# Kernel optimization log

Measured on AMD Instinct MI355X. Metric: run time of the kernel, lower is better.

Reference implementation:

```python
import jax, jax.numpy as jnp
from jax import lax
import numpy as np

D = 1024
H = 16
DK = D // 2 // H   # 32 key head dim
DV = D // H        # 64 value head dim
GATE_NORM = 16.0
SCALE = DK ** (-0.5)
EPS = 1e-5


def setup_inputs() -> dict:
    key = jax.random.key(0)
    ks = jax.random.split(key, 10)
    s = 0.02
    return {
        "inputs": jax.random.normal(ks[0], (4, 4096, D), dtype=jnp.float32),
        "Wq": jax.random.normal(ks[1], (D, D // 2), dtype=jnp.float32) * s,
        "Wk": jax.random.normal(ks[2], (D, D // 2), dtype=jnp.float32) * s,
        "Wg1": jax.random.normal(ks[3], (D, 16), dtype=jnp.float32) * s,
        "Wg2": jax.random.normal(ks[4], (16, D // 2), dtype=jnp.float32) * s,
        "Wv": jax.random.normal(ks[5], (D, D), dtype=jnp.float32) * s,
        "Wg": jax.random.normal(ks[6], (D, D), dtype=jnp.float32) * s,
        "bg": jax.random.normal(ks[7], (D,), dtype=jnp.float32) * s,
        "Wo": jax.random.normal(ks[8], (D, D), dtype=jnp.float32) * s,
    }


def _split_heads(x, dh):
    # [B, L, H*dh] -> [B, H, L, dh]
    B, L, _ = x.shape
    return x.reshape(B, L, H, dh).transpose(0, 2, 1, 3)


def _gla_scan(q, k, v, log_gate):
    # q,k,log_gate: [B,H,L,DK]; v: [B,H,L,DV]
    B = q.shape[0]
    qt = jnp.moveaxis(q, 2, 0)          # [L,B,H,DK]
    kt = jnp.moveaxis(k, 2, 0)
    vt = jnp.moveaxis(v, 2, 0)          # [L,B,H,DV]
    gt = jnp.exp(jnp.moveaxis(log_gate, 2, 0))  # [L,B,H,DK]

    def step(state, inp):
        qq, kk, vv, gg = inp
        # state: [B,H,DK,DV]
        state = state * gg[..., None] + kk[..., :, None] * vv[..., None, :]
        out = jnp.einsum('bhd,bhde->bhe', qq, state)
        return state, out

    init = jnp.zeros((B, H, DK, DV), dtype=q.dtype)
    _, outs = lax.scan(step, init, (qt, kt, vt, gt))
    return jnp.moveaxis(outs, 0, 2)     # [B,H,L,DV]


def reference(inputs, Wq, Wk, Wg1, Wg2, Wv, Wg, bg, Wo):
    B, L, _ = inputs.shape
    q = _split_heads(inputs @ Wq, DK)
    k = _split_heads((inputs @ Wk) * SCALE, DK)
    kg = _split_heads((inputs @ Wg1) @ Wg2, DK)
    v = _split_heads(inputs @ Wv, DV)
    gate = jax.nn.silu(inputs @ Wg + bg)            # [B,L,D]

    log_gate = jax.nn.log_sigmoid(kg) / GATE_NORM
    o = _gla_scan(q, k, v, log_gate)                # [B,H,L,DV]

    # group norm over value head dim (no affine)
    mu = jnp.mean(o, axis=-1, keepdims=True)
    var = jnp.var(o, axis=-1, keepdims=True)
    o = (o - mu) * lax.rsqrt(var + EPS)

    o = o.transpose(0, 2, 1, 3).reshape(B, L, D)    # b h l d -> b l (h d)
    return (gate * o) @ Wo
```

## Files before the change

### kernel.cpp

```cpp
#include <hip/hip_runtime.h>
#include <cstdint>

namespace {

constexpr int Lq  = 4096;
constexpr int Bq  = 4;
constexpr int H_  = 16;
constexpr int Mrows = Bq * Lq;
constexpr int CHK  = 64;
constexpr int NCHK = Lq / CHK;
constexpr int QKVS = 3072;
constexpr float kScale = 0.17677669529663687f;
constexpr float kEps   = 1e-5f;

typedef __attribute__((ext_vector_type(8))) short short8;
typedef __attribute__((ext_vector_type(4))) float f32x4;

__device__ __forceinline__ float bf2f(unsigned short u) {
  return __uint_as_float(((unsigned)u) << 16);
}
__device__ __forceinline__ unsigned short f2bf(float f) {
  unsigned u = __float_as_uint(f);
  u += 0x7fffu + ((u >> 16) & 1u);
  return (unsigned short)(u >> 16);
}
__device__ __forceinline__ void gload_lds16(const void* g, void* l) {
  __builtin_amdgcn_global_load_lds(
      (const __attribute__((address_space(1))) void*)g,
      (__attribute__((address_space(3))) void*)l, 16, 0, 0);
}

__global__ __launch_bounds__(256)
void cvt_bf16(const float* __restrict__ in, unsigned short* __restrict__ out, int n4)
{
  int i = blockIdx.x * 256 + threadIdx.x;
  const int stride = gridDim.x * 256;
  for (; i < n4; i += stride) {
    float4 f = ((const float4*)in)[i];
    ushort4 u = make_ushort4(f2bf(f.x), f2bf(f.y), f2bf(f.z), f2bf(f.w));
    ((ushort4*)out)[i] = u;
  }
}

struct CvtArgs {
  const float* W[5];
  unsigned short* Wt[5];
  int   N[5];
  float scale[5];
  int   start[5];
  int   nb[5];
};

__global__ __launch_bounds__(256)
void cvt_w_all(CvtArgs a)
{
  __shared__ float T[64][65];
  const int tid = threadIdx.x;
  const int b = blockIdx.x;
  int seg = 0;
  #pragma unroll
  for (int i = 1; i < 5; ++i) seg += (b >= a.start[i]) ? 1 : 0;
  const float* W = a.W[seg];
  unsigned short* Wt = a.Wt[seg];
  const int N = a.N[seg];
  const float scale = a.scale[seg];
  const int lb = b - a.start[seg];
  const int n0 = (lb % a.nb[seg]) * 64;
  const int k0 = (lb / a.nb[seg]) * 64;

  #pragma unroll
  for (int it = 0; it < 4; ++it) {
    int kr = (tid >> 4) + it * 16;
    float4 f = *(const float4*)(W + (size_t)(k0 + kr) * N + n0 + (tid & 15) * 4);
    T[kr][(tid & 15) * 4 + 0] = f.x;
    T[kr][(tid & 15) * 4 + 1] = f.y;
    T[kr][(tid & 15) * 4 + 2] = f.z;
    T[kr][(tid & 15) * 4 + 3] = f.w;
  }
  __syncthreads();
  #pragma unroll
  for (int it = 0; it < 4; ++it) {
    int nr = (tid >> 4) + it * 16;
    int c0 = (tid & 15) * 4;
    ushort4 u = make_ushort4(f2bf(T[c0 + 0][nr] * scale), f2bf(T[c0 + 1][nr] * scale),
                             f2bf(T[c0 + 2][nr] * scale), f2bf(T[c0 + 3][nr] * scale));
    *(ushort4*)(Wt + (size_t)(n0 + nr) * 1024 + k0 + c0) = u;
  }
}

template<int EPI>
__global__ __launch_bounds__(512, 1)
void gemm256(const unsigned short* __restrict__ A,
             const unsigned short* __restrict__ Bt,
             const float* __restrict__ bias,
             void* __restrict__ Cout, int N)
{
  __shared__ __align__(16) unsigned short As[2][256 * 64];
  __shared__ __align__(16) unsigned short Bs[2][256 * 64];
  const int tid = threadIdx.x;
  const int w = tid >> 6, l = tid & 63;
  const int wm = w >> 2, wn = w & 3;

  const int nbx = gridDim.x;
  const int bid = blockIdx.y * nbx + blockIdx.x;
  const int xcd = bid & 7;
  const int idx = bid >> 3;
  const int nsup = idx >> 4;
  const int rem = idx & 15;
  const int mi = rem >> 1, ni = rem & 1;
  const int m0 = (xcd * 8 + mi) * 256;
  const int n0 = (nsup * 2 + ni) * 256;

  const int srow = tid >> 3;
  const int scol = ((tid & 7) ^ ((tid >> 3) & 7)) * 8;
  const unsigned short* gAp[4];
  const unsigned short* gBp[4];
  #pragma unroll
  for (int i = 0; i < 4; ++i) {
    gAp[i] = A  + (size_t)(m0 + i * 64 + srow) * 1024 + scol;
    gBp[i] = Bt + (size_t)(n0 + i * 64 + srow) * 1024 + scol;
  }

  const int rbA = wm * 128 + (l & 15);
  const int rbB = wn * 64 + (l & 15);
  const int swzA = (rbA & 7) << 4;
  const int swzB = (rbB & 7) << 4;
  const int colb = (l >> 4) * 16;

  f32x4 acc[8][4];
  #pragma unroll
  for (int i = 0; i < 8; ++i)
    #pragma unroll
    for (int j = 0; j < 4; ++j)
      acc[i][j] = (f32x4){0.f, 0.f, 0.f, 0.f};

  #pragma unroll
  for (int i = 0; i < 4; ++i) {
    gload_lds16(gAp[i], (char*)&As[0][0] + i * 8192 + w * 1024);
    gload_lds16(gBp[i], (char*)&Bs[0][0] + i * 8192 + w * 1024);
    gAp[i] += 64; gBp[i] += 64;
  }

  int cur = 0;
  for (int t = 0; t < 16; ++t) {
    char* ldsA  = (char*)&As[cur][0];
    char* ldsB  = (char*)&Bs[cur][0];
    char* ldsAn = (char*)&As[cur ^ 1][0];
    char* ldsBn = (char*)&Bs[cur ^ 1][0];

    asm volatile("s_waitcnt vmcnt(0)" ::: "memory");
    __builtin_amdgcn_s_barrier();
    __builtin_amdgcn_sched_barrier(0);
    if (t < 15) {
      #pragma unroll
      for (int i = 0; i < 4; ++i) {
        gload_lds16(gAp[i], ldsAn + i * 8192 + w * 1024);
        gload_lds16(gBp[i], ldsBn + i * 8192 + w * 1024);
        gAp[i] += 64; gBp[i] += 64;
      }
    }

    #pragma unroll
    for (int ks = 0; ks < 2; ++ks) {
      short8 av[8], bv[4];
      #pragma unroll
      for (int mf = 0; mf < 8; ++mf) {
        int row = rbA + mf * 16;
        av[mf] = *(const short8*)(ldsA + row * 128 + ((ks * 64 + colb) ^ swzA));
      }
      #pragma unroll
      for (int nf = 0; nf < 4; ++nf) {
        int row = rbB + nf * 16;
        bv[nf] = *(const short8*)(ldsB + row * 128 + ((ks * 64 + colb) ^ swzB));
      }
      asm volatile("s_waitcnt lgkmcnt(0)" ::: "memory");
      __builtin_amdgcn_sched_barrier(0);
      __builtin_amdgcn_s_setprio(1);
      #pragma unroll
      for (int mf = 0; mf < 8; ++mf)
        #pragma unroll
        for (int nf = 0; nf < 4; ++nf)
          acc[mf][nf] = __builtin_amdgcn_mfma_f32_16x16x32_bf16(
              av[mf], bv[nf], acc[mf][nf], 0, 0, 0);
      __builtin_amdgcn_s_setprio(0);
    }
    cur ^= 1;
  }

  const int cr = (l >> 4) * 4;
  const int cc = l & 15;
  #pragma unroll
  for (int mf = 0; mf < 8; ++mf) {
    #pragma unroll
    for (int nf = 0; nf < 4; ++nf) {
      int row = m0 + wm * 128 + mf * 16 + cr;
      int col = n0 + wn * 64 + nf * 16 + cc;
      #pragma unroll
      for (int j = 0; j < 4; ++j) {
        float x = acc[mf][nf][j];
        if (EPI == 2) {
          if (col >= 2048) {
            float z = x + bias[col - 2048];
            x = z / (1.f + expf(-z));
          }
        }
        if (EPI == 3)
          ((float*)Cout)[(size_t)(row + j) * N + col] = x;
        else
          ((unsigned short*)Cout)[(size_t)(row + j) * N + col] = f2bf(x);
      }
    }
  }
}

__global__ __launch_bounds__(256)
void gemm_g1(const unsigned short* __restrict__ x, const float* __restrict__ W1,
             float* __restrict__ t1)
{
  __shared__ float Xs[16][64];
  __shared__ float Ws[64][16];
  const int tid = threadIdx.x;
  const int m0 = blockIdx.x * 16;
  const int mi = tid >> 4, n = tid & 15;
  float acc = 0.f;
  for (int k0 = 0; k0 < 1024; k0 += 64) {
    ushort4 xv = *(const ushort4*)(x + (size_t)(m0 + (tid >> 4)) * 1024 + k0 + (tid & 15) * 4);
    Xs[tid >> 4][(tid & 15) * 4 + 0] = bf2f(xv.x);
    Xs[tid >> 4][(tid & 15) * 4 + 1] = bf2f(xv.y);
    Xs[tid >> 4][(tid & 15) * 4 + 2] = bf2f(xv.z);
    Xs[tid >> 4][(tid & 15) * 4 + 3] = bf2f(xv.w);
    *(float4*)&Ws[tid >> 2][(tid & 3) * 4] =
        *(const float4*)(W1 + (size_t)(k0 + (tid >> 2)) * 16 + (tid & 3) * 4);
    __syncthreads();
    #pragma unroll
    for (int kk = 0; kk < 64; ++kk)
      acc = fmaf(Xs[mi][kk], Ws[kk][n], acc);
    __syncthreads();
  }
  t1[(size_t)(m0 + mi) * 16 + n] = acc;
}

__global__ __launch_bounds__(256)
void gemm_g2(const float* __restrict__ t1, const float* __restrict__ W2,
             float* __restrict__ lg)
{
  const int idx = blockIdx.x * 256 + threadIdx.x;
  const int m = idx >> 9, n = idx & 511;
  float acc = 0.f;
  #pragma unroll
  for (int kk = 0; kk < 16; ++kk)
    acc = fmaf(t1[m * 16 + kk], W2[kk * 512 + n], acc);
  float ls = fminf(acc, 0.f) - log1pf(expf(-fabsf(acc)));
  lg[idx] = ls * 0.0625f;
}

__global__ __launch_bounds__(256)
void gla_chunk_state(const unsigned short* __restrict__ qkv, const float* __restrict__ lg,
                     float* __restrict__ P, float* __restrict__ Dd)
{
  __shared__ __align__(16) float Lc[CHK][32];
  __shared__ float Gp[8][32];
  __shared__ __align__(16) unsigned short kdT[32][72];
  __shared__ __align__(16) unsigned short vT[64][72];
  const int blk = blockIdx.x;
  const int bh = blk >> 6, chunk = blk & (NCHK - 1);
  const int b = bh >> 4, h = bh & 15;
  const int tid = threadIdx.x;
  const int w = tid >> 6, l = tid & 63;
  const size_t rbase = ((size_t)b * Lq + (size_t)chunk * CHK) * QKVS;
  const size_t rowk = rbase + 512 + h * 32;
  const size_t rowv = rbase + 1024 + h * 64;
  const size_t rowl = ((size_t)b * Lq + (size_t)chunk * CHK) * 512 + h * 32;

  #pragma unroll
  for (int r = 0; r < 2; ++r) {
    int s4 = (tid + 256 * r) * 4;
    int t = s4 >> 5, d0 = s4 & 31;
    *(float4*)&Lc[t][d0] = *(const float4*)(lg + rowl + (size_t)t * 512 + d0);
  }
  __syncthreads();
  {
    const int d = tid & 31, g = tid >> 5;
    float v[8];
    float s = 0.f;
    #pragma unroll
    for (int i = 0; i < 8; ++i) { v[i] = Lc[g * 8 + i][d]; s += v[i]; }
    Gp[g][d] = s;
    __syncthreads();
    float run = 0.f;
    for (int i = 0; i < g; ++i) run += Gp[i][d];
    #pragma unroll
    for (int i = 0; i < 8; ++i) { run += v[i]; Lc[g * 8 + i][d] = run; }
  }
  __syncthreads();
  #pragma unroll
  for (int r = 0; r < 2; ++r) {
    int s4 = (tid + 256 * r) * 4;
    int t = s4 >> 5, d0 = s4 & 31;
    ushort4 kv = *(const ushort4*)(qkv + rowk + (size_t)t * QKVS + d0);
    float4 lc = *(const float4*)&Lc[t][d0];
    float4 ls = *(const float4*)&Lc[CHK - 1][d0];
    kdT[d0 + 0][t] = f2bf(bf2f(kv.x) * expf(ls.x - lc.x));
    kdT[d0 + 1][t] = f2bf(bf2f(kv.y) * expf(ls.y - lc.y));
    kdT[d0 + 2][t] = f2bf(bf2f(kv.z) * expf(ls.z - lc.z));
    kdT[d0 + 3][t] = f2bf(bf2f(kv.w) * expf(ls.w - lc.w));
  }
  #pragma unroll
  for (int r = 0; r < 4; ++r) {
    int s4 = (tid + 256 * r) * 4;
    int t = s4 >> 6, e0 = s4 & 63;
    ushort4 vv = *(const ushort4*)(qkv + rowv + (size_t)t * QKVS + e0);
    vT[e0 + 0][t] = vv.x;
    vT[e0 + 1][t] = vv.y;
    vT[e0 + 2][t] = vv.z;
    vT[e0 + 3][t] = vv.w;
  }
  __syncthreads();
  #pragma unroll
  for (int dj = 0; dj < 2; ++dj) {
    f32x4 acc = (f32x4){0.f, 0.f, 0.f, 0.f};
    #pragma unroll
    for (int ks = 0; ks < 2; ++ks) {
      short8 aV = *(const short8*)((const char*)&vT[0][0] +
                    (16 * w + (l & 15)) * 144 + ks * 64 + (l >> 4) * 16);
      short8 bK = *(const short8*)((const char*)&kdT[0][0] +
                    (16 * dj + (l & 15)) * 144 + ks * 64 + (l >> 4) * 16);
      acc = __builtin_amdgcn_mfma_f32_16x16x32_bf16(aV, bK, acc, 0, 0, 0);
    }
    #pragma unroll
    for (int j = 0; j < 4; ++j) {
      int e = 16 * w + (l >> 4) * 4 + j;
      int d = 16 * dj + (l & 15);
      P[(size_t)blk * 2048 + e * 32 + d] = acc[j];
    }
  }
  if (tid < 32) Dd[(size_t)blk * 32 + tid] = expf(Lc[CHK - 1][tid]);
}

__global__ __launch_bounds__(256)
void gla_chain(float* __restrict__ P, const float* __restrict__ Dd)
{
  const int bh = blockIdx.x >> 1, half = blockIdx.x & 1;
  const int tid = threadIdx.x;
  const int f = tid * 4 + half * 1024;
  const int d0 = f & 31;
  const size_t pb = (size_t)bh * NCHK;
  float4 s = {0.f, 0.f, 0.f, 0.f};

  float4 p0 = *(const float4*)(P + (pb + 0) * 2048 + f);
  float4 p1 = *(const float4*)(P + (pb + 1) * 2048 + f);
  float4 p2 = *(const float4*)(P + (pb + 2) * 2048 + f);
  float4 p3 = *(const float4*)(P + (pb + 3) * 2048 + f);
  float4 g0 = *(const float4*)(Dd + (pb + 0) * 32 + d0);
  float4 g1 = *(const float4*)(Dd + (pb + 1) * 32 + d0);
  float4 g2 = *(const float4*)(Dd + (pb + 2) * 32 + d0);
  float4 g3 = *(const float4*)(Dd + (pb + 3) * 32 + d0);

  for (int i = 0; i < NCHK; i += 4) {
    *(float4*)(P + (pb + i) * 2048 + f) = s;
    s.x = fmaf(s.x, g0.x, p0.x); s.y = fmaf(s.y, g0.y, p0.y);
    s.z = fmaf(s.z, g0.z, p0.z); s.w = fmaf(s.w, g0.w, p0.w);
    if (i + 4 < NCHK) {
      p0 = *(const float4*)(P + (pb + i + 4) * 2048 + f);
      g0 = *(const float4*)(Dd + (pb + i + 4) * 32 + d0);
    }
    *(float4*)(P + (pb + i + 1) * 2048 + f) = s;
    s.x = fmaf(s.x, g1.x, p1.x); s.y = fmaf(s.y, g1.y, p1.y);
    s.z = fmaf(s.z, g1.z, p1.z); s.w = fmaf(s.w, g1.w, p1.w);
    if (i + 5 < NCHK) {
      p1 = *(const float4*)(P + (pb + i + 5) * 2048 + f);
      g1 = *(const float4*)(Dd + (pb + i + 5) * 32 + d0);
    }
    *(float4*)(P + (pb + i + 2) * 2048 + f) = s;
    s.x = fmaf(s.x, g2.x, p2.x); s.y = fmaf(s.y, g2.y, p2.y);
    s.z = fmaf(s.z, g2.z, p2.z); s.w = fmaf(s.w, g2.w, p2.w);
    if (i + 6 < NCHK) {
      p2 = *(const float4*)(P + (pb + i + 6) * 2048 + f);
      g2 = *(const float4*)(Dd + (pb + i + 6) * 32 + d0);
    }
    *(float4*)(P + (pb + i + 3) * 2048 + f) = s;
    s.x = fmaf(s.x, g3.x, p3.x); s.y = fmaf(s.y, g3.y, p3.y);
    s.z = fmaf(s.z, g3.z, p3.z); s.w = fmaf(s.w, g3.w, p3.w);
    if (i + 7 < NCHK) {
      p3 = *(const float4*)(P + (pb + i + 7) * 2048 + f);
      g3 = *(const float4*)(Dd + (pb + i + 7) * 32 + d0);
    }
  }
}

__global__ __launch_bounds__(256)
void gla_chunk_out(const unsigned short* __restrict__ qkv, const float* __restrict__ lg,
                   const float* __restrict__ S, unsigned short* __restrict__ gated)
{
  __shared__ __align__(16) float Lc[CHK][32];
  __shared__ float Gp[8][32];
  __shared__ __align__(16) unsigned short qb[CHK][40];
  __shared__ __align__(16) unsigned short kd[CHK][40];
  __shared__ __align__(16) unsigned short vT[64][72];
  __shared__ __align__(16) unsigned short ST[64][40];
  __shared__ __align__(16) unsigned short Aq[64][72];
  const int blk = blockIdx.x;
  const int bh = blk >> 6, chunk = blk & (NCHK - 1);
  const int b = bh >> 4, h = bh & 15;
  const int tid = threadIdx.x;
  const int w = tid >> 6, l = tid & 63;
  const size_t rbase = ((size_t)b * Lq + (size_t)chunk * CHK) * QKVS;
  const size_t rowq = rbase + h * 32;
  const size_t rowk = rbase + 512 + h * 32;
  const size_t rowv = rbase + 1024 + h * 64;
  const size_t rowl = ((size_t)b * Lq + (size_t)chunk * CHK) * 512 + h * 32;

  #pragma unroll
  for (int r = 0; r < 2; ++r) {
    int s4 = (tid + 256 * r) * 4;
    int t = s4 >> 5, d0 = s4 & 31;
    *(float4*)&Lc[t][d0] = *(const float4*)(lg + rowl + (size_t)t * 512 + d0);
  }
  __syncthreads();
  {
    const int d = tid & 31, g = tid >> 5;
    float v[8];
    float s = 0.f;
    #pragma unroll
    for (int i = 0; i < 8; ++i) { v[i] = Lc[g * 8 + i][d]; s += v[i]; }
    Gp[g][d] = s;
    __syncthreads();
    float run = 0.f;
    for (int i = 0; i < g; ++i) run += Gp[i][d];
    #pragma unroll
    for (int i = 0; i < 8; ++i) { run += v[i]; Lc[g * 8 + i][d] = run; }
  }
  __syncthreads();
  #pragma unroll
  for (int r = 0; r < 2; ++r) {
    int s4 = (tid + 256 * r) * 4;
    int t = s4 >> 5, d0 = s4 & 31;
    ushort4 kv = *(const ushort4*)(qkv + rowk + (size_t)t * QKVS + d0);
    ushort4 qv = *(const ushort4*)(qkv + rowq + (size_t)t * QKVS + d0);
    float4 lc = *(const float4*)&Lc[t][d0];
    ushort4 ko, qo;
    ko.x = f2bf(bf2f(kv.x) * expf(-lc.x)); qo.x = f2bf(bf2f(qv.x) * expf(lc.x));
    ko.y = f2bf(bf2f(kv.y) * expf(-lc.y)); qo.y = f2bf(bf2f(qv.y) * expf(lc.y));
    ko.z = f2bf(bf2f(kv.z) * expf(-lc.z)); qo.z = f2bf(bf2f(qv.z) * expf(lc.z));
    ko.w = f2bf(bf2f(kv.w) * expf(-lc.w)); qo.w = f2bf(bf2f(qv.w) * expf(lc.w));
    *(ushort4*)&kd[t][d0] = ko;
    *(ushort4*)&qb[t][d0] = qo;
  }
  #pragma unroll
  for (int r = 0; r < 4; ++r) {
    int s4 = (tid + 256 * r) * 4;
    int t = s4 >> 6, e0 = s4 & 63;
    ushort4 vv = *(const ushort4*)(qkv + rowv + (size_t)t * QKVS + e0);
    vT[e0 + 0][t] = vv.x;
    vT[e0 + 1][t] = vv.y;
    vT[e0 + 2][t] = vv.z;
    vT[e0 + 3][t] = vv.w;
  }
  #pragma unroll
  for (int r = 0; r < 2; ++r) {
    int s4 = (tid + 256 * r) * 4;
    int e = s4 >> 5, d0 = s4 & 31;
    float4 f = *(const float4*)(S + (size_t)blk * 2048 + s4);
    ushort4 u = make_ushort4(f2bf(f.x), f2bf(f.y), f2bf(f.z), f2bf(f.w));
    *(ushort4*)&ST[e][d0] = u;
  }
  __syncthreads();

  short8 aQ = *(const short8*)((const char*)&qb[0][0] +
               (16 * w + (l & 15)) * 80 + (l >> 4) * 16);
  const int tl0 = (l >> 4) * 4;
  #pragma unroll
  for (int si = 0; si < 4; ++si) {
    if (si <= w) {
      short8 bK = *(const short8*)((const char*)&kd[0][0] +
                   (16 * si + (l & 15)) * 80 + (l >> 4) * 16);
      f32x4 acc = (f32x4){0.f, 0.f, 0.f, 0.f};
      acc = __builtin_amdgcn_mfma_f32_16x16x32_bf16(aQ, bK, acc, 0, 0, 0);
      #pragma unroll
      for (int j = 0; j < 4; ++j) {
        bool keep = (si < w) || ((l & 15) <= tl0 + j);
        Aq[16 * w + tl0 + j][16 * si + (l & 15)] = keep ? f2bf(acc[j]) : 0;
      }
    } else {
      #pragma unroll
      for (int j = 0; j < 4; ++j)
        Aq[16 * w + tl0 + j][16 * si + (l & 15)] = 0;
    }
  }
  __syncthreads();

  short8 aA0 = *(const short8*)((const char*)&Aq[0][0] +
                (16 * w + (l & 15)) * 144 + (l >> 4) * 16);
  short8 aA1 = *(const short8*)((const char*)&Aq[0][0] +
                (16 * w + (l & 15)) * 144 + 64 + (l >> 4) * 16);
  f32x4 accs[4];
  #pragma unroll
  for (int ej = 0; ej < 4; ++ej) {
    f32x4 acc = (f32x4){0.f, 0.f, 0.f, 0.f};
    short8 bV0 = *(const short8*)((const char*)&vT[0][0] +
                  (16 * ej + (l & 15)) * 144 + (l >> 4) * 16);
    short8 bV1 = *(const short8*)((const char*)&vT[0][0] +
                  (16 * ej + (l & 15)) * 144 + 64 + (l >> 4) * 16);
    short8 bS = *(const short8*)((const char*)&ST[0][0] +
                  (16 * ej + (l & 15)) * 80 + (l >> 4) * 16);
    acc = __builtin_amdgcn_mfma_f32_16x16x32_bf16(aA0, bV0, acc, 0, 0, 0);
    acc = __builtin_amdgcn_mfma_f32_16x16x32_bf16(aA1, bV1, acc, 0, 0, 0);
    acc = __builtin_amdgcn_mfma_f32_16x16x32_bf16(aQ,  bS,  acc, 0, 0, 0);
    accs[ej] = acc;
  }

  float mean[4], rstd[4];
  #pragma unroll
  for (int j = 0; j < 4; ++j) {
    float s  = accs[0][j] + accs[1][j] + accs[2][j] + accs[3][j];
    float q2 = accs[0][j] * accs[0][j] + accs[1][j] * accs[1][j]
             + accs[2][j] * accs[2][j] + accs[3][j] * accs[3][j];
    #pragma unroll
    for (int m = 1; m <= 8; m <<= 1) {
      s  += __shfl_xor(s, m, 64);
      q2 += __shfl_xor(q2, m, 64);
    }
    float mu = s * (1.f / 64.f);
    mean[j] = mu;
    rstd[j] = rsqrtf(q2 * (1.f / 64.f) - mu * mu + kEps);
  }

  const size_t gbase = rbase + 2048 + h * 64;
  const size_t obase = ((size_t)b * Lq + (size_t)chunk * CHK) * 1024 + h * 64;
  #pragma unroll
  for (int ej = 0; ej < 4; ++ej) {
    int e = 16 * ej + (l & 15);
    #pragma unroll
    for (int j = 0; j < 4; ++j) {
      int t = 16 * w + tl0 + j;
      float gate = bf2f(qkv[gbase + (size_t)t * QKVS + e]);
      float y = (accs[ej][j] - mean[j]) * rstd[j];
      gated[obase + (size_t)t * 1024 + e] = f2bf(gate * y);
    }
  }
}

}

extern "C" void kernel_launch(void* const* d_in, const int* in_sizes, int n_in,
                              void* d_out, int out_size, void* d_ws, size_t ws_size,
                              hipStream_t stream)
{
  (void)in_sizes; (void)n_in; (void)out_size; (void)ws_size;
  const float* x   = (const float*)d_in[0];
  const float* Wq  = (const float*)d_in[1];
  const float* Wk  = (const float*)d_in[2];
  const float* Wg1 = (const float*)d_in[3];
  const float* Wg2 = (const float*)d_in[4];
  const float* Wv  = (const float*)d_in[5];
  const float* Wg  = (const float*)d_in[6];
  const float* bg  = (const float*)d_in[7];
  const float* Wo  = (const float*)d_in[8];

  char* w = (char*)d_ws;
  unsigned short* xh   = (unsigned short*)w; w += (size_t)Mrows * 1024 * 2;
  unsigned short* qkvg = (unsigned short*)w; w += (size_t)Mrows * QKVS * 2;
  float*  lgb = (float*)w;                   w += (size_t)Mrows * 512 * 4;
  float*  t1  = (float*)w;                   w += (size_t)Mrows * 16 * 4;
  float*  Pst = (float*)w;                   w += (size_t)64 * NCHK * 2048 * 4;
  float*  Dd  = (float*)w;                   w += (size_t)64 * NCHK * 32 * 4;
  unsigned short* Wqkvgt = (unsigned short*)w; w += (size_t)QKVS * 1024 * 2;
  unsigned short* Wot    = (unsigned short*)w; w += (size_t)1024 * 1024 * 2;
  unsigned short* gated  = xh;

  cvt_bf16<<<2048, 256, 0, stream>>>(x, xh, Mrows * 1024 / 4);
  CvtArgs ca;
  ca.W[0] = Wq;  ca.Wt[0] = Wqkvgt;                        ca.N[0] = 512;  ca.scale[0] = 1.f;    ca.start[0] = 0;   ca.nb[0] = 8;
  ca.W[1] = Wk;  ca.Wt[1] = Wqkvgt + (size_t)512 * 1024;   ca.N[1] = 512;  ca.scale[1] = kScale; ca.start[1] = 128; ca.nb[1] = 8;
  ca.W[2] = Wv;  ca.Wt[2] = Wqkvgt + (size_t)1024 * 1024;  ca.N[2] = 1024; ca.scale[2] = 1.f;    ca.start[2] = 256; ca.nb[2] = 16;
  ca.W[3] = Wg;  ca.Wt[3] = Wqkvgt + (size_t)2048 * 1024;  ca.N[3] = 1024; ca.scale[3] = 1.f;    ca.start[3] = 512; ca.nb[3] = 16;
  ca.W[4] = Wo;  ca.Wt[4] = Wot;                           ca.N[4] = 1024; ca.scale[4] = 1.f;    ca.start[4] = 768; ca.nb[4] = 16;
  cvt_w_all<<<1024, 256, 0, stream>>>(ca);
  gemm256<2><<<dim3(12, 64), 512, 0, stream>>>(xh, Wqkvgt, bg, qkvg, QKVS);
  gemm_g1<<<Mrows / 16, 256, 0, stream>>>(xh, Wg1, t1);
  gemm_g2<<<(Mrows * 512) / 256, 256, 0, stream>>>(t1, Wg2, lgb);
  gla_chunk_state<<<64 * NCHK, 256, 0, stream>>>(qkvg, lgb, Pst, Dd);
  gla_chain<<<128, 256, 0, stream>>>(Pst, Dd);
  gla_chunk_out<<<64 * NCHK, 256, 0, stream>>>(qkvg, lgb, Pst, gated);
  gemm256<3><<<dim3(4, 64), 512, 0, stream>>>(gated, Wot, nullptr, d_out, 1024);
}
```

Measured before the change: 344.3 us.

## Switch GEMM to four-stage K=32 LDS ring with three loads in flight

The 256x256 GEMM previously double-buffered K=64 tiles and waited for all outstanding global-to-LDS loads each iteration. It now uses a four-slot ring of K=32 tiles, keeping up to three tiles in flight with partial vmcnt waits. It also uses a new XOR swizzle suited to 64-byte rows. The aim is to hide global memory latency better. The cost is twice as many barriers per K, and the barrier count per MFMA block doubles.

```diff
diff --git a/kernel.cpp b/kernel.cpp
--- a/kernel.cpp
+++ b/kernel.cpp
@@ -95,8 +95,7 @@
              const float* __restrict__ bias,
              void* __restrict__ Cout, int N)
 {
-  __shared__ __align__(16) unsigned short As[2][256 * 64];
-  __shared__ __align__(16) unsigned short Bs[2][256 * 64];
+  __shared__ __align__(16) unsigned short Buf[4][16384];
   const int tid = threadIdx.x;
   const int w = tid >> 6, l = tid & 63;
   const int wm = w >> 2, wn = w & 3;
@@ -111,21 +110,16 @@
   const int m0 = (xcd * 8 + mi) * 256;
   const int n0 = (nsup * 2 + ni) * 256;
 
-  const int srow = tid >> 3;
-  const int scol = ((tid & 7) ^ ((tid >> 3) & 7)) * 8;
-  const unsigned short* gAp[4];
-  const unsigned short* gBp[4];
-  #pragma unroll
-  for (int i = 0; i < 4; ++i) {
-    gAp[i] = A  + (size_t)(m0 + i * 64 + srow) * 1024 + scol;
-    gBp[i] = Bt + (size_t)(n0 + i * 64 + srow) * 1024 + scol;
-  }
+  const int srow = tid >> 2;
+  const int scol = ((tid & 3) ^ ((tid >> 3) & 3)) * 8;
+  const unsigned short* gA0 = A  + (size_t)(m0 + srow) * 1024 + scol;
+  const unsigned short* gA1 = A  + (size_t)(m0 + 128 + srow) * 1024 + scol;
+  const unsigned short* gB0 = Bt + (size_t)(n0 + srow) * 1024 + scol;
+  const unsigned short* gB1 = Bt + (size_t)(n0 + 128 + srow) * 1024 + scol;
 
   const int rbA = wm * 128 + (l & 15);
   const int rbB = wn * 64 + (l & 15);
-  const int swzA = (rbA & 7) << 4;
-  const int swzB = (rbB & 7) << 4;
-  const int colb = (l >> 4) * 16;
+  const int sw = (((((l & 15) >> 1) & 3) ^ (l >> 4)) << 4);
 
   f32x4 acc[8][4];
   #pragma unroll
@@ -135,56 +129,50 @@
       acc[i][j] = (f32x4){0.f, 0.f, 0.f, 0.f};
 
   #pragma unroll
-  for (int i = 0; i < 4; ++i) {
-    gload_lds16(gAp[i], (char*)&As[0][0] + i * 8192 + w * 1024);
-    gload_lds16(gBp[i], (char*)&Bs[0][0] + i * 8192 + w * 1024);
-    gAp[i] += 64; gBp[i] += 64;
-  }
-
-  int cur = 0;
-  for (int t = 0; t < 16; ++t) {
-    char* ldsA  = (char*)&As[cur][0];
-    char* ldsB  = (char*)&Bs[cur][0];
-    char* ldsAn = (char*)&As[cur ^ 1][0];
-    char* ldsBn = (char*)&Bs[cur ^ 1][0];
-
-    asm volatile("s_waitcnt vmcnt(0)" ::: "memory");
+  for (int h = 0; h < 3; ++h) {
+    char* dst = (char*)&Buf[h][0] + w * 1024;
+    gload_lds16(gA0, dst);
+    gload_lds16(gA1, dst + 8192);
+    gload_lds16(gB0, dst + 16384);
+    gload_lds16(gB1, dst + 24576);
+    gA0 += 32; gA1 += 32; gB0 += 32; gB1 += 32;
+  }
+
+  for (int h = 0; h < 32; ++h) {
+    if (h < 30)       asm volatile("s_waitcnt vmcnt(8)" ::: "memory");
+    else if (h == 30) asm volatile("s_waitcnt vmcnt(4)" ::: "memory");
+    else              asm volatile("s_waitcnt vmcnt(0)" ::: "memory");
     __builtin_amdgcn_s_barrier();
     __builtin_amdgcn_sched_barrier(0);
-    if (t < 15) {
+
+    if (h + 3 < 32) {
+      char* dst = (char*)&Buf[(h + 3) & 3][0] + w * 1024;
+      gload_lds16(gA0, dst);
+      gload_lds16(gA1, dst + 8192);
+      gload_lds16(gB0, dst + 16384);
+      gload_lds16(gB1, dst + 24576);
+      gA0 += 32; gA1 += 32; gB0 += 32; gB1 += 32;
+    }
+
+    char* ldsA = (char*)&Buf[h & 3][0];
+    char* ldsB = ldsA + 16384;
+    short8 av[8], bv[4];
+    #pragma unroll
+    for (int mf = 0; mf < 8; ++mf)
+      av[mf] = *(const short8*)(ldsA + (rbA + mf * 16) * 64 + sw);
+    #pragma unroll
+    for (int nf = 0; nf < 4; ++nf)
+      bv[nf] = *(const short8*)(ldsB + (rbB + nf * 16) * 64 + sw);
+    asm volatile("s_waitcnt lgkmcnt(0)" ::: "memory");
+    __builtin_amdgcn_sched_barrier(0);
+    __builtin_amdgcn_s_setprio(1);
+    #pragma unroll
+    for (int mf = 0; mf < 8; ++mf)
       #pragma unroll
-      for (int i = 0; i < 4; ++i) {
-        gload_lds16(gAp[i], ldsAn + i * 8192 + w * 1024);
-        gload_lds16(gBp[i], ldsBn + i * 8192 + w * 1024);
-        gAp[i] += 64; gBp[i] += 64;
-      }
-    }
-
-    #pragma unroll
-    for (int ks = 0; ks < 2; ++ks) {
-      short8 av[8], bv[4];
-      #pragma unroll
-      for (int mf = 0; mf < 8; ++mf) {
-        int row = rbA + mf * 16;
-        av[mf] = *(const short8*)(ldsA + row * 128 + ((ks * 64 + colb) ^ swzA));
-      }
-      #pragma unroll
-      for (int nf = 0; nf < 4; ++nf) {
-        int row = rbB + nf * 16;
-        bv[nf] = *(const short8*)(ldsB + row * 128 + ((ks * 64 + colb) ^ swzB));
-      }
-      asm volatile("s_waitcnt lgkmcnt(0)" ::: "memory");
-      __builtin_amdgcn_sched_barrier(0);
-      __builtin_amdgcn_s_setprio(1);
-      #pragma unroll
-      for (int mf = 0; mf < 8; ++mf)
-        #pragma unroll
-        for (int nf = 0; nf < 4; ++nf)
-          acc[mf][nf] = __builtin_amdgcn_mfma_f32_16x16x32_bf16(
-              av[mf], bv[nf], acc[mf][nf], 0, 0, 0);
-      __builtin_amdgcn_s_setprio(0);
-    }
-    cur ^= 1;
+      for (int nf = 0; nf < 4; ++nf)
+        acc[mf][nf] = __builtin_amdgcn_mfma_f32_16x16x32_bf16(
+            av[mf], bv[nf], acc[mf][nf], 0, 0, 0);
+    __builtin_amdgcn_s_setprio(0);
   }
 
   const int cr = (l >> 4) * 4;
```

Result: faster. 330.9 us (-3.9%).
